# Optimization experiments

Hardware: AMD Instinct MI355X
Metric: run time of the kernel (lower is better)

The kernel has to match this reference:

```python
import jax, jax.numpy as jnp
import numpy as np

N_NODES_PER_GRAPH = 16
N_GRAPHS = 256
D = 512


def _build_graph(n=N_NODES_PER_GRAPH, B=N_GRAPHS):
    # fully-connected directed graph (no self loops) per sample, DGL insertion order
    ii, jj = np.meshgrid(np.arange(n), np.arange(n), indexing='ij')
    m = ii != jj
    s, d = ii[m], jj[m]                     # [n*(n-1)] src-major order
    offs = (np.arange(B) * n)[:, None]
    src = (s[None, :] + offs).reshape(-1)
    dst = (d[None, :] + offs).reshape(-1)
    E_g = n * (n - 1)
    # target->other edges are (0, dst) for dst in 1..n-1 => first n-1 eids of each graph
    t_o_eid = ((np.arange(B) * E_g)[:, None] + np.arange(n - 1)[None, :]).reshape(-1)
    return src.astype(np.int32), dst.astype(np.int32), t_o_eid.astype(np.int32)


def setup_inputs() -> dict:
    key = jax.random.key(0)
    n, B, d = N_NODES_PER_GRAPH, N_GRAPHS, D
    N = n * B
    src, dst, t_o_eid = _build_graph(n, B)
    E = src.shape[0]
    ks = jax.random.split(key, 6)
    sc = 0.02
    return {
        'visual_feat': jax.random.normal(ks[0], (N, d), jnp.float32),
        'spatial_feat': jax.random.normal(ks[1], (E, d), jnp.float32),
        'W_edge': jax.random.normal(ks[2], (3 * d, d), jnp.float32) * sc,
        'b_edge': jnp.zeros((d,), jnp.float32),
        'W_attn': jax.random.normal(ks[3], (d, 1), jnp.float32) * sc,
        'b_attn': jnp.zeros((1,), jnp.float32),
        'W_node': jax.random.normal(ks[4], (2 * d, d), jnp.float32) * sc,
        'b_node': jnp.zeros((d,), jnp.float32),
        'W_pred': jax.random.normal(ks[5], (3 * d, d), jnp.float32) * sc,
        'b_pred': jnp.zeros((d,), jnp.float32),
        'src': jnp.asarray(src),
        'dst': jnp.asarray(dst),
        't_o_eid': jnp.asarray(t_o_eid),
    }


def reference(visual_feat, spatial_feat, W_edge, b_edge, W_attn, b_attn,
              W_node, b_node, W_pred, b_pred, src, dst, t_o_eid):
    N = visual_feat.shape[0]
    # EdgeApplyModule: gather src/dst node feats, concat with spatial, MLP
    efeat = jnp.concatenate([visual_feat[src], spatial_feat, visual_feat[dst]], axis=1)  # [E,3D]
    e_f = jax.nn.relu(efeat @ W_edge + b_edge)                        # [E,D]
    # EdgeAttentionApplyModule: scalar attention logit per edge
    a = jax.nn.relu(e_f @ W_attn + b_attn)[:, 0]                      # [E]
    # reduce: softmax over incoming-edge mailbox per dst node (segment softmax)
    a_max = jax.ops.segment_max(a, dst, num_segments=N)
    ex = jnp.exp(a - a_max[dst])
    denom = jax.ops.segment_sum(ex, dst, num_segments=N)
    alpha = ex / denom[dst]                                           # [E]
    msg = visual_feat[src] + e_f                                      # old_n_f + e_f
    z_f = jax.ops.segment_sum(alpha[:, None] * msg, dst, num_segments=N)  # [N,D]
    # NodeApplyModule: concat(n_f, z_f) -> MLP
    new_n_f = jax.nn.relu(jnp.concatenate([visual_feat, z_f], axis=1) @ W_node + b_node)
    # interaction predictor on target->other edges
    ts, td = src[t_o_eid], dst[t_o_eid]
    pfeat = jnp.concatenate([new_n_f[ts], spatial_feat[t_o_eid], new_n_f[td]], axis=1)
    pred = jax.nn.relu(pfeat @ W_pred + b_pred)                       # [E_to, D]
    return pred
```

## Files before the change

kernel.cpp:

```cpp
#include <hip/hip_runtime.h>
#include <hip/hip_bf16.h>
#include <stdint.h>

#define BM 128
#define BN 128

typedef __attribute__((ext_vector_type(8))) short bf16x8;
typedef __attribute__((ext_vector_type(4))) float f32x4;
typedef __attribute__((ext_vector_type(4))) uint32_t u32x4;

__device__ __forceinline__ uint32_t pk2(float lo, float hi) {
  union { __hip_bfloat162 h; uint32_t u; } un;
  un.h = __float22bfloat162_rn(make_float2(lo, hi));
  return un.u;
}
__device__ __forceinline__ uint16_t bfc(float f) {
  return (uint16_t)(pk2(f, f) & 0xFFFFu);
}
__device__ __forceinline__ float bf2f(uint16_t s) {
  union { uint32_t u; float f; } v; v.u = ((uint32_t)s) << 16;
  return v.f;
}
__device__ __forceinline__ void gload_lds16(const void* g, void* l) {
  __builtin_amdgcn_global_load_lds((const __attribute__((address_space(1))) void*)g,
                                   (__attribute__((address_space(3))) void*)l, 16, 0, 0);
}
__device__ __forceinline__ int xcd_swz(int d, int n) {
  const int q = n >> 3, r = n & 7, x = d & 7, i = d >> 3;
  return (x < r ? x * (q + 1) : r * (q + 1) + (x - r) * q) + i;
}

enum { E_PLAIN16 = 0, E_EDGE = 1, E_NODE = 2, E_PRED = 3 };

struct GemmArgs {
  const uint16_t* Ab; int lda;
  const float* Af;
  const int* gidx;
  const uint16_t* B0;
  const uint16_t* B1;
  int K;
  int nwg, ncol;
  const float* cvt_src;
  uint16_t* cvt_dst;
  uint16_t* C16; int ldc;
  const float* bias;
  const float* wattn;
  const int* src; const int* dst; const int* toe;
  const uint16_t* A13;
  const uint16_t* U13;
  uint16_t* EF;
  float* AATT;
  float* OUT;
};

template <int EPI>
__device__ __forceinline__ void gemm_epilogue(const GemmArgs& g, f32x4 (&acc)[4][2],
                                              int m0, int n0g, int wm, int wn,
                                              int lr, int lg, int vb, const short* a13s) {
  const int rbase = m0 + wm * 64;
  const int cbase = n0g + wn * 32;
  if constexpr (EPI == E_PLAIN16) {
#pragma unroll
    for (int m = 0; m < 4; ++m)
#pragma unroll
      for (int r = 0; r < 4; ++r) {
        const int row = rbase + m * 16 + lg * 4 + r;
#pragma unroll
        for (int n = 0; n < 2; ++n)
          g.C16[(size_t)row * g.ldc + cbase + n * 16 + lr] = bfc(acc[m][n][r]);
      }
  } else if constexpr (EPI == E_NODE) {
#pragma unroll
    for (int m = 0; m < 4; ++m)
#pragma unroll
      for (int r = 0; r < 4; ++r) {
        const int row = rbase + m * 16 + lg * 4 + r;
#pragma unroll
        for (int n = 0; n < 2; ++n) {
          const int col = cbase + n * 16 + lr;
          g.C16[(size_t)row * g.ldc + col] = bfc(fmaxf(acc[m][n][r] + g.bias[col], 0.f));
        }
      }
  } else if constexpr (EPI == E_EDGE) {
    float bv[2], wv[2]; int lc[2];
#pragma unroll
    for (int n = 0; n < 2; ++n) {
      lc[n] = wn * 32 + n * 16 + lr;
      bv[n] = g.bias[n0g + lc[n]];
      wv[n] = g.wattn[n0g + lc[n]];
    }
#pragma unroll
    for (int m = 0; m < 4; ++m)
#pragma unroll
      for (int r = 0; r < 4; ++r) {
        const int e = rbase + m * 16 + lg * 4 + r;
        const int se = g.src[e] - vb, de = g.dst[e] - vb;
        float rp = 0.f;
#pragma unroll
        for (int n = 0; n < 2; ++n) {
          float v = acc[m][n][r] + bf2f((uint16_t)a13s[se * 256 + lc[n]]) +
                    bf2f((uint16_t)a13s[de * 256 + 128 + lc[n]]) + bv[n];
          v = fmaxf(v, 0.f);
          rp += v * wv[n];
          g.EF[(size_t)e * 512 + n0g + lc[n]] = bfc(v);
        }
        for (int d = 1; d < 16; d <<= 1) rp += __shfl_xor(rp, d);
        if (lr == 0) atomicAdd(&g.AATT[e], rp);
      }
  } else {
    float bv[2]; int cols[2];
#pragma unroll
    for (int n = 0; n < 2; ++n) { cols[n] = cbase + n * 16 + lr; bv[n] = g.bias[cols[n]]; }
#pragma unroll
    for (int m = 0; m < 4; ++m)
#pragma unroll
      for (int r = 0; r < 4; ++r) {
        const int row = rbase + m * 16 + lg * 4 + r;
        const int te = g.toe[row];
        const int ts = g.src[te], td = g.dst[te];
        const uint16_t* u1 = g.U13 + (size_t)ts * 1024;
        const uint16_t* u3 = g.U13 + (size_t)td * 1024 + 512;
#pragma unroll
        for (int n = 0; n < 2; ++n) {
          const float v = acc[m][n][r] + bf2f(u1[cols[n]]) + bf2f(u3[cols[n]]) + bv[n];
          g.OUT[(size_t)row * 512 + cols[n]] = fmaxf(v, 0.f);
        }
      }
  }
}

template <int EPI>
__global__ __launch_bounds__(512, 6) void gemm_lds_k(GemmArgs g) {
  __shared__ __align__(16) short As[8192];
  __shared__ __align__(16) short Bs[8192];
  __shared__ __align__(16) short a13s[(EPI == E_EDGE) ? 8192 : 16];
  const int tid = threadIdx.x, w = tid >> 6, lane = tid & 63;

  if ((int)blockIdx.x >= g.nwg) {
    const size_t base = ((size_t)(blockIdx.x - g.nwg) * 512 + tid) * 16;
#pragma unroll
    for (int rr = 0; rr < 2; ++rr) {
      const size_t b2 = base + rr * 8;
      const float4 f0 = *(const float4*)(g.cvt_src + b2);
      const float4 f1 = *(const float4*)(g.cvt_src + b2 + 4);
      u32x4 u;
      u[0] = pk2(f0.x, f0.y); u[1] = pk2(f0.z, f0.w);
      u[2] = pk2(f1.x, f1.y); u[3] = pk2(f1.z, f1.w);
      *(u32x4*)(g.cvt_dst + b2) = u;
    }
    return;
  }

  const int sid = xcd_swz(blockIdx.x, g.nwg);
  const int colb = sid % g.ncol, rowb = sid / g.ncol;
  const int m0 = rowb * BM, n0g = colb * BN;

  const uint16_t* Bp = g.B0; int n0 = n0g;
  if (n0g >= 512) { Bp = g.B1; n0 = n0g - 512; }

  const int r1 = w * 8 + (lane >> 3);
  const int sc = ((lane & 7) ^ ((lane >> 3) & 7)) * 8;
  const int d1 = w * 512 + lane * 8;
  const uint16_t* gB1 = Bp + (size_t)(n0 + r1) * g.K + sc;
  const uint16_t* gB2 = Bp + (size_t)(n0 + r1 + 64) * g.K + sc;
  int ga1 = m0 + r1, ga2 = m0 + r1 + 64;
  if (g.gidx) { ga1 = g.gidx[ga1]; ga2 = g.gidx[ga2]; }
  const uint16_t* gA1 = g.Ab + (size_t)ga1 * g.lda + sc;
  const uint16_t* gA2 = g.Ab + (size_t)ga2 * g.lda + sc;

  int vb = 0;
  if constexpr (EPI == E_EDGE) {
    vb = (m0 / 240) * 16;
#pragma unroll
    for (int rd = 0; rd < 2; ++rd) {
      const int idx = rd * 512 + tid;
      const int node = idx >> 5, chunk = idx & 31;
      const int colg = (chunk < 16) ? (n0g + chunk * 8) : (512 + n0g + (chunk - 16) * 8);
      gload_lds16(g.A13 + (size_t)(vb + node) * 1024 + colg, &a13s[idx * 8]);
    }
  }

  const int wm = w >> 2, wn = w & 3;
  const int lr = lane & 15, lg = lane >> 4;
  int aro[2][4], bro[2][2];
#pragma unroll
  for (int h = 0; h < 2; ++h) {
    const int pc = ((h * 4 + lg) ^ (lr & 7)) * 8;
#pragma unroll
    for (int m = 0; m < 4; ++m) aro[h][m] = (wm * 64 + m * 16 + lr) * 64 + pc;
#pragma unroll
    for (int n = 0; n < 2; ++n) bro[h][n] = (wn * 32 + n * 16 + lr) * 64 + pc;
  }

  f32x4 acc[4][2] = {};

  for (int k0 = 0; k0 < g.K; k0 += 64) {
    __syncthreads();
    gload_lds16(gB1 + k0, &Bs[d1]);
    gload_lds16(gB2 + k0, &Bs[d1 + 4096]);
    gload_lds16(gA1 + k0, &As[d1]);
    gload_lds16(gA2 + k0, &As[d1 + 4096]);
    __syncthreads();
#pragma unroll
    for (int h = 0; h < 2; ++h) {
      bf16x8 av[4], bv[2];
#pragma unroll
      for (int m = 0; m < 4; ++m) av[m] = *(const bf16x8*)&As[aro[h][m]];
#pragma unroll
      for (int n = 0; n < 2; ++n) bv[n] = *(const bf16x8*)&Bs[bro[h][n]];
#pragma unroll
      for (int m = 0; m < 4; ++m)
#pragma unroll
        for (int n = 0; n < 2; ++n)
          acc[m][n] = __builtin_amdgcn_mfma_f32_16x16x32_bf16(av[m], bv[n], acc[m][n], 0, 0, 0);
    }
  }

  gemm_epilogue<EPI>(g, acc, m0, n0g, wm, wn, lr, lg, vb, a13s);
}

template <int EPI>
__global__ __launch_bounds__(512, 4) void gemm_reg_k(GemmArgs g) {
  __shared__ __align__(16) short As[4096];
  __shared__ __align__(16) short Bs[4096];
  __shared__ __align__(16) short a13s[(EPI == E_EDGE) ? 8192 : 16];
  const int tid = threadIdx.x, w = tid >> 6, lane = tid & 63;
  const int sid = xcd_swz(blockIdx.x, g.nwg);
  const int colb = sid % g.ncol, rowb = sid / g.ncol;
  const int m0 = rowb * BM, n0g = colb * BN;
  const uint16_t* Bp = g.B0; int n0 = n0g;
  if (n0g >= 512) { Bp = g.B1; n0 = n0g - 512; }
  const int gr = tid >> 2, gk = (tid & 3) * 8;
  const uint16_t* gB = Bp + (size_t)(n0 + gr) * g.K + gk;
  const int sofs = gr * 32 + gk;
  int ra = m0 + gr;
  if (g.gidx) ra = g.gidx[ra];
  const float* arow = g.Af + (size_t)ra * 512 + gk;
  int vb = 0;
  if constexpr (EPI == E_EDGE) {
    vb = (m0 / 240) * 16;
#pragma unroll
    for (int rd = 0; rd < 2; ++rd) {
      const int idx = rd * 512 + tid;
      const int node = idx >> 5, chunk = idx & 31;
      const int colg = (chunk < 16) ? (n0g + chunk * 8) : (512 + n0g + (chunk - 16) * 8);
      gload_lds16(g.A13 + (size_t)(vb + node) * 1024 + colg, &a13s[idx * 8]);
    }
  }
  const int wm = w >> 2, wn = w & 3;
  const int lr = lane & 15, lg = lane >> 4;
  int aro[4], bro[2];
#pragma unroll
  for (int m = 0; m < 4; ++m) aro[m] = (wm * 64 + m * 16 + lr) * 32 + lg * 8;
#pragma unroll
  for (int n = 0; n < 2; ++n) bro[n] = (wn * 32 + n * 16 + lr) * 32 + lg * 8;
  f32x4 acc[4][2] = {};
  for (int k0 = 0; k0 < g.K; k0 += 32) {
    __syncthreads();
    gload_lds16(gB + k0, &Bs[sofs]);
    const float4 f0 = *(const float4*)(arow + k0);
    const float4 f1 = *(const float4*)(arow + k0 + 4);
    u32x4 q;
    q[0] = pk2(f0.x, f0.y); q[1] = pk2(f0.z, f0.w);
    q[2] = pk2(f1.x, f1.y); q[3] = pk2(f1.z, f1.w);
    *(u32x4*)&As[sofs] = q;
    __syncthreads();
    bf16x8 av[4], bv[2];
#pragma unroll
    for (int m = 0; m < 4; ++m) av[m] = *(const bf16x8*)&As[aro[m]];
#pragma unroll
    for (int n = 0; n < 2; ++n) bv[n] = *(const bf16x8*)&Bs[bro[n]];
#pragma unroll
    for (int m = 0; m < 4; ++m)
#pragma unroll
      for (int n = 0; n < 2; ++n)
        acc[m][n] = __builtin_amdgcn_mfma_f32_16x16x32_bf16(av[m], bv[n], acc[m][n], 0, 0, 0);
  }
  gemm_epilogue<EPI>(g, acc, m0, n0g, wm, wn, lr, lg, vb, a13s);
}

__global__ __launch_bounds__(256) void prep_k(const float* vis, const float* We,
                                              const float* Wn, const float* Wp,
                                              uint16_t* VISB, uint16_t* NIN,
                                              uint16_t* WT, float* AATT) {
  __shared__ float tile[32][33];
  const int b = blockIdx.x, tid = threadIdx.x;
  if (b < 1024) {
    const int base = (b * 256 + tid) * 8;
    const int row = base >> 9, col = base & 511;
    const float4 f0 = *(const float4*)(vis + base);
    const float4 f1 = *(const float4*)(vis + base + 4);
    u32x4 u;
    u[0] = pk2(f0.x, f0.y); u[1] = pk2(f0.z, f0.w);
    u[2] = pk2(f1.x, f1.y); u[3] = pk2(f1.z, f1.w);
    *(u32x4*)(VISB + base) = u;
    *(u32x4*)(NIN + (size_t)row * 1024 + col) = u;
  } else if (b < 3072) {
    const int zb = b - 1024, z = zb >> 8, rem = zb & 255;
    const float* srcp; uint16_t* dstp; int ldo = 512, koff = 0;
    switch (z) {
      default:
      case 0: srcp = We;          dstp = WT;           break;
      case 1: srcp = We + 262144; dstp = WT + 262144;  break;
      case 2: srcp = We + 524288; dstp = WT + 524288;  break;
      case 3: srcp = Wn;          dstp = WT + 786432;  ldo = 1024; break;
      case 4: srcp = Wn + 262144; dstp = WT + 786432;  ldo = 1024; koff = 512; break;
      case 5: srcp = Wp;          dstp = WT + 1310720; break;
      case 6: srcp = Wp + 262144; dstp = WT + 1572864; break;
      case 7: srcp = Wp + 524288; dstp = WT + 1835008; break;
    }
    const int kb = (rem & 15) * 32, nb = (rem >> 4) * 32;
    const int tx = tid & 31, ty = tid >> 5;
#pragma unroll
    for (int s = 0; s < 4; ++s)
      tile[ty + 8 * s][tx] = srcp[(size_t)(kb + ty + 8 * s) * 512 + nb + tx];
    __syncthreads();
#pragma unroll
    for (int s = 0; s < 4; ++s) {
      const int n = nb + ty + 8 * s, k = kb + tx;
      dstp[(size_t)n * ldo + koff + k] = bfc(tile[tx][ty + 8 * s]);
    }
  } else {
    const int i = (b - 3072) * 1024 + tid * 4;
    float4 z4; z4.x = z4.y = z4.z = z4.w = 0.f;
    *(float4*)(AATT + i) = z4;
  }
}

__global__ __launch_bounds__(256) void node_reduce_k(const float* AATT, const float* battn,
                                                     const uint16_t* EF, const uint16_t* VISB,
                                                     uint16_t* NIN) {
  const int sub = threadIdx.x >> 7;
  const int t = threadIdx.x & 127;
  const int v = blockIdx.x * 2 + sub;
  const int gph = v >> 4, j = v & 15;
  __shared__ float sa_s[2][16];
  __shared__ float alf_s[2][16];
  __shared__ int eids_s[2][16];
  __shared__ int srcs_s[2][16];
  if (t < 15) {
    const int i = (t < j) ? t : t + 1;
    const int off = (j < i) ? j : (j - 1);
    const int eid = gph * 240 + i * 15 + off;
    eids_s[sub][t] = eid;
    srcs_s[sub][t] = gph * 16 + i;
    sa_s[sub][t] = fmaxf(AATT[eid] + battn[0], 0.f);
  }
  __syncthreads();
  float mx = -1e30f;
#pragma unroll
  for (int i = 0; i < 15; ++i) mx = fmaxf(mx, sa_s[sub][i]);
  float den = 0.f;
#pragma unroll
  for (int i = 0; i < 15; ++i) den += expf(sa_s[sub][i] - mx);
  if (t < 15) alf_s[sub][t] = expf(sa_s[sub][t] - mx) / den;
  __syncthreads();
  const int c = t * 4;
  float z0 = 0.f, z1 = 0.f, z2 = 0.f, z3 = 0.f;
#pragma unroll
  for (int i = 0; i < 15; ++i) {
    const float a = alf_s[sub][i];
    const ushort4 e4 = *(const ushort4*)(EF + (size_t)eids_s[sub][i] * 512 + c);
    const ushort4 v4 = *(const ushort4*)(VISB + (size_t)srcs_s[sub][i] * 512 + c);
    z0 += a * (bf2f(e4.x) + bf2f(v4.x)); z1 += a * (bf2f(e4.y) + bf2f(v4.y));
    z2 += a * (bf2f(e4.z) + bf2f(v4.z)); z3 += a * (bf2f(e4.w) + bf2f(v4.w));
  }
  ushort4 o;
  o.x = bfc(z0); o.y = bfc(z1); o.z = bfc(z2); o.w = bfc(z3);
  *(ushort4*)(NIN + (size_t)v * 1024 + 512 + c) = o;
}

extern "C" void kernel_launch(void* const* d_in, const int* in_sizes, int n_in,
                              void* d_out, int out_size, void* d_ws, size_t ws_size,
                              hipStream_t stream) {
  const float* visual = (const float*)d_in[0];
  const float* spatial = (const float*)d_in[1];
  const float* W_edge = (const float*)d_in[2];
  const float* b_edge = (const float*)d_in[3];
  const float* W_attn = (const float*)d_in[4];
  const float* b_attn = (const float*)d_in[5];
  const float* W_node = (const float*)d_in[6];
  const float* b_node = (const float*)d_in[7];
  const float* W_pred = (const float*)d_in[8];
  const float* b_pred = (const float*)d_in[9];
  const int* src = (const int*)d_in[10];
  const int* dst = (const int*)d_in[11];
  const int* toe = (const int*)d_in[12];
  float* out = (float*)d_out;

  char* ws = (char*)d_ws;
  uint16_t* WT = (uint16_t*)ws;
  uint16_t* VISB = (uint16_t*)(ws + 4194304);
  uint16_t* NIN = (uint16_t*)(ws + 8388608);
  uint16_t* A13b = (uint16_t*)(ws + 16777216);
  uint16_t* EF = (uint16_t*)(ws + 25165824);
  float* AATT = (float*)(ws + 88080384);
  uint16_t* SPB = (uint16_t*)(ws + 88326144);
  const bool spb_ok = ws_size >= 151240704ull;
  uint16_t* U13b = A13b;
  uint16_t* NNF = EF;

  prep_k<<<3132, 256, 0, stream>>>(visual, W_edge, W_node, W_pred, VISB, NIN, WT, AATT);

  const dim3 blk(512);
  {
    GemmArgs a = {};
    a.Ab = VISB; a.lda = 512; a.B0 = WT; a.B1 = WT + 524288; a.K = 512;
    a.nwg = 256; a.ncol = 8;
    a.C16 = A13b; a.ldc = 1024;
    int grid = 256;
    if (spb_ok) { a.cvt_src = spatial; a.cvt_dst = SPB; grid = 256 + 3840; }
    gemm_lds_k<E_PLAIN16><<<grid, blk, 0, stream>>>(a);
  }
  {
    GemmArgs a = {};
    a.B0 = WT + 262144; a.K = 512;
    a.nwg = 1920; a.ncol = 4;
    a.bias = b_edge; a.wattn = W_attn;
    a.src = src; a.dst = dst; a.A13 = A13b; a.EF = EF; a.AATT = AATT;
    if (spb_ok) {
      a.Ab = SPB; a.lda = 512;
      gemm_lds_k<E_EDGE><<<1920, blk, 0, stream>>>(a);
    } else {
      a.Af = spatial;
      gemm_reg_k<E_EDGE><<<1920, blk, 0, stream>>>(a);
    }
  }
  node_reduce_k<<<2048, 256, 0, stream>>>(AATT, b_attn, EF, VISB, NIN);
  {
    GemmArgs a = {};
    a.Ab = NIN; a.lda = 1024; a.B0 = WT + 786432; a.K = 1024;
    a.nwg = 128; a.ncol = 4;
    a.bias = b_node; a.C16 = NNF; a.ldc = 512;
    gemm_lds_k<E_NODE><<<128, blk, 0, stream>>>(a);
  }
  {
    GemmArgs a = {};
    a.Ab = NNF; a.lda = 512; a.B0 = WT + 1310720; a.B1 = WT + 1835008; a.K = 512;
    a.nwg = 256; a.ncol = 8;
    a.C16 = U13b; a.ldc = 1024;
    gemm_lds_k<E_PLAIN16><<<256, blk, 0, stream>>>(a);
  }
  {
    GemmArgs a = {};
    a.B0 = WT + 1572864; a.K = 512;
    a.nwg = 120; a.ncol = 4;
    a.bias = b_pred; a.toe = toe; a.src = src; a.dst = dst; a.U13 = U13b; a.OUT = out;
    a.gidx = toe;
    if (spb_ok) {
      a.Ab = SPB; a.lda = 512;
      gemm_lds_k<E_PRED><<<120, blk, 0, stream>>>(a);
    } else {
      a.Af = spatial;
      gemm_reg_k<E_PRED><<<120, blk, 0, stream>>>(a);
    }
  }
  (void)in_sizes; (void)n_in; (void)out_size;
}
```

Baseline: 179.5 us.

## Fold source-node features into edge epilogue and reuse GEMM LDS tiles

The edge GEMM epilogue now adds the bf16 source-node visual feature to the activated edge feature before storing, so the node reduction reads one pre-summed message per edge instead of two gathers. The separate a13s shared buffer is dropped, and the A13/VISB side data is loaded into the GEMM's As/Bs tiles after the K loop. This cuts LDS per block and raises the launch-bounds occupancy hint from 6 to 8. The trade-off is that the side-data load is no longer overlapped with the main loop, and the message is rounded to bf16 after the add.

```diff
diff --git a/kernel.cpp b/kernel.cpp
--- a/kernel.cpp
+++ b/kernel.cpp
@@ -47,6 +47,7 @@
   const float* wattn;
   const int* src; const int* dst; const int* toe;
   const uint16_t* A13;
+  const uint16_t* VISB;
   const uint16_t* U13;
   uint16_t* EF;
   float* AATT;
@@ -56,7 +57,8 @@
 template <int EPI>
 __device__ __forceinline__ void gemm_epilogue(const GemmArgs& g, f32x4 (&acc)[4][2],
                                               int m0, int n0g, int wm, int wn,
-                                              int lr, int lg, int vb, const short* a13s) {
+                                              int lr, int lg, int vb,
+                                              const short* a13s, const short* viss) {
   const int rbase = m0 + wm * 64;
   const int cbase = n0g + wn * 32;
   if constexpr (EPI == E_PLAIN16) {
@@ -102,7 +104,8 @@
                     bf2f((uint16_t)a13s[de * 256 + 128 + lc[n]]) + bv[n];
           v = fmaxf(v, 0.f);
           rp += v * wv[n];
-          g.EF[(size_t)e * 512 + n0g + lc[n]] = bfc(v);
+          g.EF[(size_t)e * 512 + n0g + lc[n]] =
+              bfc(v + bf2f((uint16_t)viss[se * 128 + lc[n]]));
         }
         for (int d = 1; d < 16; d <<= 1) rp += __shfl_xor(rp, d);
         if (lr == 0) atomicAdd(&g.AATT[e], rp);
@@ -130,10 +133,9 @@
 }
 
 template <int EPI>
-__global__ __launch_bounds__(512, 6) void gemm_lds_k(GemmArgs g) {
+__global__ __launch_bounds__(512, 8) void gemm_lds_k(GemmArgs g) {
   __shared__ __align__(16) short As[8192];
   __shared__ __align__(16) short Bs[8192];
-  __shared__ __align__(16) short a13s[(EPI == E_EDGE) ? 8192 : 16];
   const int tid = threadIdx.x, w = tid >> 6, lane = tid & 63;
 
   if ((int)blockIdx.x >= g.nwg) {
@@ -168,62 +170,68 @@
   const uint16_t* gA1 = g.Ab + (size_t)ga1 * g.lda + sc;
   const uint16_t* gA2 = g.Ab + (size_t)ga2 * g.lda + sc;
 
-  int vb = 0;
+  const int vb = (EPI == E_EDGE) ? (m0 / 240) * 16 : 0;
+
+  const int wm = w >> 2, wn = w & 3;
+  const int lr = lane & 15, lg = lane >> 4;
+  int aro[2][4], bro[2][2];
+#pragma unroll
+  for (int h = 0; h < 2; ++h) {
+    const int pc = ((h * 4 + lg) ^ (lr & 7)) * 8;
+#pragma unroll
+    for (int m = 0; m < 4; ++m) aro[h][m] = (wm * 64 + m * 16 + lr) * 64 + pc;
+#pragma unroll
+    for (int n = 0; n < 2; ++n) bro[h][n] = (wn * 32 + n * 16 + lr) * 64 + pc;
+  }
+
+  f32x4 acc[4][2] = {};
+
+  for (int k0 = 0; k0 < g.K; k0 += 64) {
+    __syncthreads();
+    gload_lds16(gB1 + k0, &Bs[d1]);
+    gload_lds16(gB2 + k0, &Bs[d1 + 4096]);
+    gload_lds16(gA1 + k0, &As[d1]);
+    gload_lds16(gA2 + k0, &As[d1 + 4096]);
+    __syncthreads();
+#pragma unroll
+    for (int h = 0; h < 2; ++h) {
+      bf16x8 av[4], bv[2];
+#pragma unroll
+      for (int m = 0; m < 4; ++m) av[m] = *(const bf16x8*)&As[aro[h][m]];
+#pragma unroll
+      for (int n = 0; n < 2; ++n) bv[n] = *(const bf16x8*)&Bs[bro[h][n]];
+#pragma unroll
+      for (int m = 0; m < 4; ++m)
+#pragma unroll
+        for (int n = 0; n < 2; ++n)
+          acc[m][n] = __builtin_amdgcn_mfma_f32_16x16x32_bf16(av[m], bv[n], acc[m][n], 0, 0, 0);
+    }
+  }
+
   if constexpr (EPI == E_EDGE) {
-    vb = (m0 / 240) * 16;
+    __syncthreads();
 #pragma unroll
     for (int rd = 0; rd < 2; ++rd) {
       const int idx = rd * 512 + tid;
       const int node = idx >> 5, chunk = idx & 31;
       const int colg = (chunk < 16) ? (n0g + chunk * 8) : (512 + n0g + (chunk - 16) * 8);
-      gload_lds16(g.A13 + (size_t)(vb + node) * 1024 + colg, &a13s[idx * 8]);
-    }
-  }
-
-  const int wm = w >> 2, wn = w & 3;
-  const int lr = lane & 15, lg = lane >> 4;
-  int aro[2][4], bro[2][2];
-#pragma unroll
-  for (int h = 0; h < 2; ++h) {
-    const int pc = ((h * 4 + lg) ^ (lr & 7)) * 8;
-#pragma unroll
-    for (int m = 0; m < 4; ++m) aro[h][m] = (wm * 64 + m * 16 + lr) * 64 + pc;
-#pragma unroll
-    for (int n = 0; n < 2; ++n) bro[h][n] = (wn * 32 + n * 16 + lr) * 64 + pc;
-  }
-
-  f32x4 acc[4][2] = {};
-
-  for (int k0 = 0; k0 < g.K; k0 += 64) {
-    __syncthreads();
-    gload_lds16(gB1 + k0, &Bs[d1]);
-    gload_lds16(gB2 + k0, &Bs[d1 + 4096]);
-    gload_lds16(gA1 + k0, &As[d1]);
-    gload_lds16(gA2 + k0, &As[d1 + 4096]);
-    __syncthreads();
-#pragma unroll
-    for (int h = 0; h < 2; ++h) {
-      bf16x8 av[4], bv[2];
-#pragma unroll
-      for (int m = 0; m < 4; ++m) av[m] = *(const bf16x8*)&As[aro[h][m]];
-#pragma unroll
-      for (int n = 0; n < 2; ++n) bv[n] = *(const bf16x8*)&Bs[bro[h][n]];
-#pragma unroll
-      for (int m = 0; m < 4; ++m)
-#pragma unroll
-        for (int n = 0; n < 2; ++n)
-          acc[m][n] = __builtin_amdgcn_mfma_f32_16x16x32_bf16(av[m], bv[n], acc[m][n], 0, 0, 0);
-    }
-  }
-
-  gemm_epilogue<EPI>(g, acc, m0, n0g, wm, wn, lr, lg, vb, a13s);
+      gload_lds16(g.A13 + (size_t)(vb + node) * 1024 + colg, &As[idx * 8]);
+    }
+    {
+      const int node = tid >> 4, chunk = tid & 15;
+      gload_lds16(g.VISB + (size_t)(vb + node) * 512 + n0g + chunk * 8, &Bs[tid * 8]);
+    }
+    __syncthreads();
+  }
+
+  gemm_epilogue<EPI>(g, acc, m0, n0g, wm, wn, lr, lg, vb, As, Bs);
 }
 
 template <int EPI>
 __global__ __launch_bounds__(512, 4) void gemm_reg_k(GemmArgs g) {
   __shared__ __align__(16) short As[4096];
   __shared__ __align__(16) short Bs[4096];
-  __shared__ __align__(16) short a13s[(EPI == E_EDGE) ? 8192 : 16];
+  __shared__ __align__(16) short axv[(EPI == E_EDGE) ? 12288 : 16];
   const int tid = threadIdx.x, w = tid >> 6, lane = tid & 63;
   const int sid = xcd_swz(blockIdx.x, g.nwg);
   const int colb = sid % g.ncol, rowb = sid / g.ncol;
@@ -244,7 +252,11 @@
       const int idx = rd * 512 + tid;
       const int node = idx >> 5, chunk = idx & 31;
       const int colg = (chunk < 16) ? (n0g + chunk * 8) : (512 + n0g + (chunk - 16) * 8);
-      gload_lds16(g.A13 + (size_t)(vb + node) * 1024 + colg, &a13s[idx * 8]);
+      gload_lds16(g.A13 + (size_t)(vb + node) * 1024 + colg, &axv[idx * 8]);
+    }
+    {
+      const int node = tid >> 4, chunk = tid & 15;
+      gload_lds16(g.VISB + (size_t)(vb + node) * 512 + n0g + chunk * 8, &axv[8192 + tid * 8]);
     }
   }
   const int wm = w >> 2, wn = w & 3;
@@ -276,7 +288,7 @@
       for (int n = 0; n < 2; ++n)
         acc[m][n] = __builtin_amdgcn_mfma_f32_16x16x32_bf16(av[m], bv[n], acc[m][n], 0, 0, 0);
   }
-  gemm_epilogue<EPI>(g, acc, m0, n0g, wm, wn, lr, lg, vb, a13s);
+  gemm_epilogue<EPI>(g, acc, m0, n0g, wm, wn, lr, lg, vb, axv, axv + 8192);
 }
 
 __global__ __launch_bounds__(256) void prep_k(const float* vis, const float* We,
@@ -328,8 +340,7 @@
 }
 
 __global__ __launch_bounds__(256) void node_reduce_k(const float* AATT, const float* battn,
-                                                     const uint16_t* EF, const uint16_t* VISB,
-                                                     uint16_t* NIN) {
+                                                     const uint16_t* MSG, uint16_t* NIN) {
   const int sub = threadIdx.x >> 7;
   const int t = threadIdx.x & 127;
   const int v = blockIdx.x * 2 + sub;
@@ -337,13 +348,11 @@
   __shared__ float sa_s[2][16];
   __shared__ float alf_s[2][16];
   __shared__ int eids_s[2][16];
-  __shared__ int srcs_s[2][16];
   if (t < 15) {
     const int i = (t < j) ? t : t + 1;
     const int off = (j < i) ? j : (j - 1);
     const int eid = gph * 240 + i * 15 + off;
     eids_s[sub][t] = eid;
-    srcs_s[sub][t] = gph * 16 + i;
     sa_s[sub][t] = fmaxf(AATT[eid] + battn[0], 0.f);
   }
   __syncthreads();
@@ -360,10 +369,9 @@
 #pragma unroll
   for (int i = 0; i < 15; ++i) {
     const float a = alf_s[sub][i];
-    const ushort4 e4 = *(const ushort4*)(EF + (size_t)eids_s[sub][i] * 512 + c);
-    const ushort4 v4 = *(const ushort4*)(VISB + (size_t)srcs_s[sub][i] * 512 + c);
-    z0 += a * (bf2f(e4.x) + bf2f(v4.x)); z1 += a * (bf2f(e4.y) + bf2f(v4.y));
-    z2 += a * (bf2f(e4.z) + bf2f(v4.z)); z3 += a * (bf2f(e4.w) + bf2f(v4.w));
+    const ushort4 e4 = *(const ushort4*)(MSG + (size_t)eids_s[sub][i] * 512 + c);
+    z0 += a * bf2f(e4.x); z1 += a * bf2f(e4.y);
+    z2 += a * bf2f(e4.z); z3 += a * bf2f(e4.w);
   }
   ushort4 o;
   o.x = bfc(z0); o.y = bfc(z1); o.z = bfc(z2); o.w = bfc(z3);
@@ -417,7 +425,7 @@
     a.B0 = WT + 262144; a.K = 512;
     a.nwg = 1920; a.ncol = 4;
     a.bias = b_edge; a.wattn = W_attn;
-    a.src = src; a.dst = dst; a.A13 = A13b; a.EF = EF; a.AATT = AATT;
+    a.src = src; a.dst = dst; a.A13 = A13b; a.VISB = VISB; a.EF = EF; a.AATT = AATT;
     if (spb_ok) {
       a.Ab = SPB; a.lda = 512;
       gemm_lds_k<E_EDGE><<<1920, blk, 0, stream>>>(a);
@@ -426,7 +434,7 @@
       gemm_reg_k<E_EDGE><<<1920, blk, 0, stream>>>(a);
     }
   }
-  node_reduce_k<<<2048, 256, 0, stream>>>(AATT, b_attn, EF, VISB, NIN);
+  node_reduce_k<<<2048, 256, 0, stream>>>(AATT, b_attn, EF, NIN);
   {
     GemmArgs a = {};
     a.Ab = NIN; a.lda = 1024; a.B0 = WT + 786432; a.K = 1024;
```

New measurement: 185.9 us. 1.04x slower.
